# Kernel tuning notes

Hardware: AMD Instinct MI355X
Metric: run time of the kernel (lower is better)

The kernel has to match this reference:

```python
import jax, jax.numpy as jnp
import numpy as np

B = 2048
LF = 64
N_DEC, N_MOV, N_CAT, N_PER, N_COM = 12, 60000, 32, 100000, 20000


def setup_inputs() -> dict:
    key = jax.random.key(0)
    ks = jax.random.split(key, 10)

    def multihot(k, n):
        return jax.random.randint(k, (B, n), 0, 2, dtype=jnp.int32)

    def weight(k, n):
        # nn.Linear(n, LF, bias=False) weight, stored transposed as [n, LF]
        return jax.random.normal(k, (n, LF), dtype=jnp.float32) * 0.02

    return {
        "decade_idxs": multihot(ks[0], N_DEC),
        "movie_idxs": multihot(ks[1], N_MOV),
        "category_idxs": multihot(ks[2], N_CAT),
        "person_idxs": multihot(ks[3], N_PER),
        "company_idxs": multihot(ks[4], N_COM),
        "W_dec": weight(ks[5], N_DEC),
        "W_mov": weight(ks[6], N_MOV),
        "W_cat": weight(ks[7], N_CAT),
        "W_per": weight(ks[8], N_PER),
        "W_com": weight(ks[9], N_COM),
    }


def _norm_rows(emb, s):
    # divide rows whose multi-hot sum s is nonzero (np.flatnonzero semantics)
    mask = s != 0
    safe = jnp.where(mask, s, jnp.ones_like(s))
    return jnp.where(mask[:, None], emb / safe[:, None], emb)


def reference(decade_idxs, movie_idxs, category_idxs, person_idxs, company_idxs,
              W_dec, W_mov, W_cat, W_per, W_com):
    d = decade_idxs.astype(jnp.float32)
    m = movie_idxs.astype(jnp.float32)
    c = category_idxs.astype(jnp.float32)
    p = person_idxs.astype(jnp.float32)
    q = company_idxs.astype(jnp.float32)

    decades = d @ W_dec            # [B, LF]
    decades = _norm_rows(decades, jnp.sum(d, axis=1))

    movies = m @ W_mov
    # BUG in original module (replicated faithfully): `decades` is normalized
    # AGAIN by the movie-row sums; `movies` is never normalized.
    decades = _norm_rows(decades, jnp.sum(m, axis=1))

    categories = _norm_rows(c @ W_cat, jnp.sum(c, axis=1))
    persons = _norm_rows(p @ W_per, jnp.sum(p, axis=1))
    companies = _norm_rows(q @ W_com, jnp.sum(q, axis=1))

    return jnp.concatenate([decades, movies, categories, persons, companies], axis=1)
```

## Files before the change

kernel.cpp:

```cpp
#include <hip/hip_runtime.h>
#include <hip/hip_bf16.h>

#define BM 128
#define BK 64
#define CHUNK 4096
#define LF 64
#define NBAGS 5
#define BROWS 2048
#define OUTC 320

typedef __attribute__((ext_vector_type(8))) short short8;
typedef __attribute__((ext_vector_type(4))) float f32x4;

struct BagArgs {
    const int*   A[NBAGS];
    const float* W[NBAGS];
    int K[NBAGS];
    int cstart[NBAGS + 1];
};

__device__ __forceinline__ unsigned short f2bf(float f) {
    unsigned u = __float_as_uint(f);
    u += 0x7FFFu + ((u >> 16) & 1u);
    return (unsigned short)(u >> 16);
}

__global__ __launch_bounds__(256) void bag_gemm(BagArgs args,
                                                float* __restrict__ out,
                                                int* __restrict__ sums) {
    __shared__ unsigned short lsA[BM * BK];
    __shared__ unsigned short lsB[LF * BK];

    const int tid  = threadIdx.x;
    const int wave = tid >> 6;
    const int lane = tid & 63;

    int y = blockIdx.y;
    int bag = 0;
#pragma unroll
    for (int b = 1; b < NBAGS; ++b)
        if (y >= args.cstart[b]) bag = b;
    const int chunk = y - args.cstart[bag];
    const int K     = args.K[bag];
    const int k0    = chunk * CHUNK;
    const int kend  = min(k0 + CHUNK, K);
    const int m0    = blockIdx.x * BM;
    const int*   __restrict__ A = args.A[bag];
    const float* __restrict__ W = args.W[bag];

    f32x4 acc[2][4];
#pragma unroll
    for (int i = 0; i < 2; ++i)
#pragma unroll
        for (int j = 0; j < 4; ++j)
            acc[i][j] = (f32x4){0.f, 0.f, 0.f, 0.f};

    const int ar = tid >> 2;
    const int aj = tid & 3;
    const int wk = tid & 63;
    const int wc0 = (tid >> 6) * 16;

    int sum0 = 0, sum1 = 0;

    for (int kk = k0; kk < kend; kk += BK) {
#pragma unroll
        for (int half = 0; half < 2; ++half) {
            const int r = ar + half * 64;
            const size_t rowoff = (size_t)(m0 + r) * (size_t)K;
#pragma unroll
            for (int i = 0; i < 4; ++i) {
                const int col = kk + aj * 4 + i * 16;
                int4 v = make_int4(0, 0, 0, 0);
                if (col < kend) v = *(const int4*)(A + rowoff + col);
                const int s = v.x + v.y + v.z + v.w;
                if (half == 0) sum0 += s; else sum1 += s;
                unsigned p0 = (v.x ? 0x3F80u : 0u) | (v.y ? 0x3F800000u : 0u);
                unsigned p1 = (v.z ? 0x3F80u : 0u) | (v.w ? 0x3F800000u : 0u);
                int kbyte = (aj * 4 + i * 16) * 2;
                kbyte ^= (r & 7) << 4;
                *(uint2*)((char*)lsA + r * (BK * 2) + kbyte) = make_uint2(p0, p1);
            }
        }
        {
            const int gk = kk + wk;
#pragma unroll
            for (int u = 0; u < 4; ++u) {
                float4 w = make_float4(0.f, 0.f, 0.f, 0.f);
                if (gk < kend) w = *(const float4*)(W + (size_t)gk * LF + wc0 + u * 4);
                const unsigned short b0 = f2bf(w.x), b1 = f2bf(w.y),
                                     b2 = f2bf(w.z), b3 = f2bf(w.w);
                const unsigned short bs[4] = {b0, b1, b2, b3};
#pragma unroll
                for (int v2 = 0; v2 < 4; ++v2) {
                    const int c = wc0 + u * 4 + v2;
                    const int kbyte = (wk * 2) ^ ((c & 7) << 4);
                    *(unsigned short*)((char*)lsB + c * (BK * 2) + kbyte) = bs[v2];
                }
            }
        }
        __syncthreads();

        const int fr   = lane & 15;
        const int kgrp = lane >> 4;
#pragma unroll
        for (int kh = 0; kh < 2; ++kh) {
            const int kbyteR = kh * 64 + kgrp * 16;
            short8 afr[2];
#pragma unroll
            for (int mi = 0; mi < 2; ++mi) {
                const int row = wave * 32 + mi * 16 + fr;
                const int off = row * (BK * 2) + (kbyteR ^ ((row & 7) << 4));
                afr[mi] = *(const short8*)((const char*)lsA + off);
            }
#pragma unroll
            for (int ni = 0; ni < 4; ++ni) {
                const int colB = ni * 16 + fr;
                const int offb = colB * (BK * 2) + (kbyteR ^ ((colB & 7) << 4));
                const short8 bfr = *(const short8*)((const char*)lsB + offb);
#pragma unroll
                for (int mi = 0; mi < 2; ++mi)
                    acc[mi][ni] = __builtin_amdgcn_mfma_f32_16x16x32_bf16(
                        afr[mi], bfr, acc[mi][ni], 0, 0, 0);
            }
        }
        __syncthreads();
    }

    sum0 += __shfl_xor(sum0, 1);
    sum0 += __shfl_xor(sum0, 2);
    sum1 += __shfl_xor(sum1, 1);
    sum1 += __shfl_xor(sum1, 2);
    if (aj == 0) {
        atomicAdd(&sums[bag * BROWS + m0 + ar], sum0);
        atomicAdd(&sums[bag * BROWS + m0 + ar + 64], sum1);
    }

    const int fr = lane & 15;
    const int rg = lane >> 4;
#pragma unroll
    for (int mi = 0; mi < 2; ++mi)
#pragma unroll
        for (int ni = 0; ni < 4; ++ni)
#pragma unroll
            for (int r = 0; r < 4; ++r) {
                const int row = m0 + wave * 32 + mi * 16 + rg * 4 + r;
                const int col = bag * LF + ni * 16 + fr;
                atomicAdd(&out[row * OUTC + col], acc[mi][ni][r]);
            }
}

__global__ __launch_bounds__(256) void norm_fix(float* __restrict__ out,
                                                const int* __restrict__ sums) {
    const int idx = blockIdx.x * blockDim.x + threadIdx.x;
    if (idx >= BROWS * OUTC) return;
    const int m = idx / OUTC;
    const int c = idx % OUTC;
    const int bag = c >> 6;
    float v = out[idx];
    if (bag == 0) {
        const int s0 = sums[m];
        const int s1 = sums[BROWS + m];
        if (s0) v /= (float)s0;
        if (s1) v /= (float)s1;
    } else if (bag >= 2) {
        const int s = sums[bag * BROWS + m];
        if (s) v /= (float)s;
    }
    out[idx] = v;
}

extern "C" void kernel_launch(void* const* d_in, const int* in_sizes, int n_in,
                              void* d_out, int out_size, void* d_ws, size_t ws_size,
                              hipStream_t stream) {
    float* out = (float*)d_out;
    int* sums = (int*)d_ws;

    hipMemsetAsync(d_out, 0, (size_t)out_size * sizeof(float), stream);
    hipMemsetAsync(sums, 0, NBAGS * BROWS * sizeof(int), stream);

    BagArgs args;
    const int Ks[NBAGS] = {12, 60000, 32, 100000, 20000};
    int total = 0;
    for (int b = 0; b < NBAGS; ++b) {
        args.A[b] = (const int*)d_in[b];
        args.W[b] = (const float*)d_in[5 + b];
        args.K[b] = Ks[b];
        args.cstart[b] = total;
        total += (Ks[b] + CHUNK - 1) / CHUNK;
    }
    args.cstart[NBAGS] = total;

    dim3 grid(BROWS / BM, total);
    bag_gemm<<<grid, 256, 0, stream>>>(args, out, sums);

    const int n = BROWS * OUTC;
    norm_fix<<<(n + 255) / 256, 256, 0, stream>>>(out, sums);
}
```

Before: 494.8 us.

## Prepack weights to bf16 tiles, load A directly into registers, double-buffer LDS

```diff
diff --git a/kernel.cpp b/kernel.cpp
--- a/kernel.cpp
+++ b/kernel.cpp
@@ -1,13 +1,14 @@
 #include <hip/hip_runtime.h>
 #include <hip/hip_bf16.h>
 
-#define BM 128
-#define BK 64
-#define CHUNK 4096
 #define LF 64
 #define NBAGS 5
 #define BROWS 2048
 #define OUTC 320
+#define CHUNK 2048
+#define BM 64
+#define BK 64
+#define WS_SUMS_BYTES 65536
 
 typedef __attribute__((ext_vector_type(8))) short short8;
 typedef __attribute__((ext_vector_type(4))) float f32x4;
@@ -17,6 +18,7 @@
     const float* W[NBAGS];
     int K[NBAGS];
     int cstart[NBAGS + 1];
+    int tstart[NBAGS + 1];
 };
 
 __device__ __forceinline__ unsigned short f2bf(float f) {
@@ -25,128 +27,167 @@
     return (unsigned short)(u >> 16);
 }
 
-__global__ __launch_bounds__(256) void bag_gemm(BagArgs args,
-                                                float* __restrict__ out,
-                                                int* __restrict__ sums) {
-    __shared__ unsigned short lsA[BM * BK];
-    __shared__ unsigned short lsB[LF * BK];
+__device__ __forceinline__ unsigned ones2(int x, int y) {
+    return (x ? 0x3F80u : 0u) | (y ? 0x3F800000u : 0u);
+}
+
+__global__ __launch_bounds__(256) void pack_w(BagArgs args,
+                                              unsigned short* __restrict__ Wp) {
+    __shared__ unsigned short ls[4][4096];
+    const int wv = threadIdx.x >> 6;
+    const int c  = threadIdx.x & 63;
+    const int gtile = blockIdx.x * 4 + wv;
+
+    int bag = 0;
+#pragma unroll
+    for (int b = 1; b < NBAGS; ++b)
+        if (gtile >= args.tstart[b]) bag = b;
+    const int lt = gtile - args.tstart[bag];
+    const float* __restrict__ W = args.W[bag];
+    const int K = args.K[bag];
+
+    unsigned short* L = ls[wv];
+#pragma unroll 8
+    for (int k = 0; k < 64; ++k) {
+        const int gk = lt * 64 + k;
+        float v = (gk < K) ? W[(size_t)gk * LF + c] : 0.f;
+        L[(((k >> 3) * LF) + c) * 8 + (k & 7)] = f2bf(v);
+    }
+    __syncthreads();
+    unsigned short* dst = Wp + ((size_t)gtile << 12);
+#pragma unroll
+    for (int j = 0; j < 8; ++j)
+        *(short8*)(dst + c * 8 + j * 512) = *(const short8*)(L + c * 8 + j * 512);
+}
+
+template<bool PACKED>
+__global__ __launch_bounds__(256, 4) void bag_gemm(BagArgs args,
+                                                   const unsigned short* __restrict__ Wp,
+                                                   float* __restrict__ out,
+                                                   int* __restrict__ sums)
+{
+    __shared__ unsigned short lsB[2][BK * LF];
 
     const int tid  = threadIdx.x;
     const int wave = tid >> 6;
     const int lane = tid & 63;
-
-    int y = blockIdx.y;
-    int bag = 0;
+    const int fr   = lane & 15;
+    const int kg   = lane >> 4;
+
+    int y = blockIdx.y, bag = 0;
 #pragma unroll
     for (int b = 1; b < NBAGS; ++b)
         if (y >= args.cstart[b]) bag = b;
-    const int chunk = y - args.cstart[bag];
-    const int K     = args.K[bag];
-    const int k0    = chunk * CHUNK;
-    const int kend  = min(k0 + CHUNK, K);
-    const int m0    = blockIdx.x * BM;
-    const int*   __restrict__ A = args.A[bag];
+    const int chunk  = y - args.cstart[bag];
+    const int K      = args.K[bag];
+    const int k0     = chunk * CHUNK;
+    const int kend   = min(k0 + CHUNK, K);
+    const int niters = (kend - k0 + BK - 1) >> 6;
+    const int tile0  = args.tstart[bag] + chunk * (CHUNK / BK);
+
+    const int m0  = blockIdx.x * BM;
+    const int row = m0 + wave * 16 + fr;
+    const int* __restrict__ pA = args.A[bag] + (size_t)row * K;
     const float* __restrict__ W = args.W[bag];
 
-    f32x4 acc[2][4];
-#pragma unroll
-    for (int i = 0; i < 2; ++i)
-#pragma unroll
-        for (int j = 0; j < 4; ++j)
-            acc[i][j] = (f32x4){0.f, 0.f, 0.f, 0.f};
-
-    const int ar = tid >> 2;
-    const int aj = tid & 3;
-    const int wk = tid & 63;
-    const int wc0 = (tid >> 6) * 16;
-
-    int sum0 = 0, sum1 = 0;
-
-    for (int kk = k0; kk < kend; kk += BK) {
-#pragma unroll
-        for (int half = 0; half < 2; ++half) {
-            const int r = ar + half * 64;
-            const size_t rowoff = (size_t)(m0 + r) * (size_t)K;
-#pragma unroll
-            for (int i = 0; i < 4; ++i) {
-                const int col = kk + aj * 4 + i * 16;
-                int4 v = make_int4(0, 0, 0, 0);
-                if (col < kend) v = *(const int4*)(A + rowoff + col);
-                const int s = v.x + v.y + v.z + v.w;
-                if (half == 0) sum0 += s; else sum1 += s;
-                unsigned p0 = (v.x ? 0x3F80u : 0u) | (v.y ? 0x3F800000u : 0u);
-                unsigned p1 = (v.z ? 0x3F80u : 0u) | (v.w ? 0x3F800000u : 0u);
-                int kbyte = (aj * 4 + i * 16) * 2;
-                kbyte ^= (r & 7) << 4;
-                *(uint2*)((char*)lsA + r * (BK * 2) + kbyte) = make_uint2(p0, p1);
+    f32x4 acc[4];
+#pragma unroll
+    for (int i = 0; i < 4; ++i) acc[i] = (f32x4){0.f, 0.f, 0.f, 0.f};
+    int psum = 0;
+
+    auto loadA = [&](int t, int4& x0, int4& x1, int4& x2, int4& x3) {
+        const int c0 = k0 + t * BK + kg * 8;
+        const int c1 = c0 + 32;
+        const int4 z = make_int4(0, 0, 0, 0);
+        x0 = (c0     < kend) ? *(const int4*)(pA + c0)     : z;
+        x1 = (c0 + 4 < kend) ? *(const int4*)(pA + c0 + 4) : z;
+        x2 = (c1     < kend) ? *(const int4*)(pA + c1)     : z;
+        x3 = (c1 + 4 < kend) ? *(const int4*)(pA + c1 + 4) : z;
+    };
+
+    auto stageW = [&](int t, int buf) {
+        if constexpr (PACKED) {
+            const char* src = (const char*)Wp + (((size_t)(tile0 + t)) << 13)
+                              + wave * 2048 + lane * 16;
+            char* dst = (char*)&lsB[buf][0] + wave * 2048;
+            __builtin_amdgcn_global_load_lds(
+                (const __attribute__((address_space(1))) void*)src,
+                (__attribute__((address_space(3))) void*)dst, 16, 0, 0);
+            __builtin_amdgcn_global_load_lds(
+                (const __attribute__((address_space(1))) void*)(src + 1024),
+                (__attribute__((address_space(3))) void*)(dst + 1024), 16, 0, 0);
+        } else {
+            const int kq = tid >> 4, cg = tid & 15;
+#pragma unroll
+            for (int u = 0; u < 4; ++u) {
+                const int k  = kq * 4 + u;
+                const int gk = k0 + t * BK + k;
+                float4 w = make_float4(0.f, 0.f, 0.f, 0.f);
+                if (gk < kend) w = *(const float4*)(W + (size_t)gk * LF + cg * 4);
+                unsigned short* d = &lsB[buf][(((k >> 3) * LF) + cg * 4) * 8 + (k & 7)];
+                d[0]  = f2bf(w.x);
+                d[8]  = f2bf(w.y);
+                d[16] = f2bf(w.z);
+                d[24] = f2bf(w.w);
             }
         }
-        {
-            const int gk = kk + wk;
-#pragma unroll
-            for (int u = 0; u < 4; ++u) {
-                float4 w = make_float4(0.f, 0.f, 0.f, 0.f);
-                if (gk < kend) w = *(const float4*)(W + (size_t)gk * LF + wc0 + u * 4);
-                const unsigned short b0 = f2bf(w.x), b1 = f2bf(w.y),
-                                     b2 = f2bf(w.z), b3 = f2bf(w.w);
-                const unsigned short bs[4] = {b0, b1, b2, b3};
-#pragma unroll
-                for (int v2 = 0; v2 < 4; ++v2) {
-                    const int c = wc0 + u * 4 + v2;
-                    const int kbyte = (wk * 2) ^ ((c & 7) << 4);
-                    *(unsigned short*)((char*)lsB + c * (BK * 2) + kbyte) = bs[v2];
-                }
-            }
-        }
+    };
+
+    int4 a0, a1, a2, a3;
+    loadA(0, a0, a1, a2, a3);
+    stageW(0, 0);
+    if constexpr (PACKED) asm volatile("s_waitcnt vmcnt(0)" ::: "memory");
+    __syncthreads();
+
+    for (int t = 0; t < niters; ++t) {
+        const int cur = t & 1;
+        int4 n0, n1, n2, n3;
+        if (t + 1 < niters) {
+            loadA(t + 1, n0, n1, n2, n3);
+            stageW(t + 1, cur ^ 1);
+        } else {
+            n0 = n1 = n2 = n3 = make_int4(0, 0, 0, 0);
+        }
+
+        psum += a0.x + a0.y + a0.z + a0.w + a1.x + a1.y + a1.z + a1.w
+              + a2.x + a2.y + a2.z + a2.w + a3.x + a3.y + a3.z + a3.w;
+
+        int4 u0 = make_int4(ones2(a0.x, a0.y), ones2(a0.z, a0.w),
+                            ones2(a1.x, a1.y), ones2(a1.z, a1.w));
+        int4 u1 = make_int4(ones2(a2.x, a2.y), ones2(a2.z, a2.w),
+                            ones2(a3.x, a3.y), ones2(a3.z, a3.w));
+        short8 fa0 = *(short8*)&u0;
+        short8 fa1 = *(short8*)&u1;
+
+        const unsigned short* Lb = &lsB[cur][0];
+#pragma unroll
+        for (int ni = 0; ni < 4; ++ni) {
+            short8 fb = *(const short8*)(Lb + ((0 * 4 + kg) * LF + ni * 16 + fr) * 8);
+            acc[ni] = __builtin_amdgcn_mfma_f32_16x16x32_bf16(fa0, fb, acc[ni], 0, 0, 0);
+        }
+#pragma unroll
+        for (int ni = 0; ni < 4; ++ni) {
+            short8 fb = *(const short8*)(Lb + ((1 * 4 + kg) * LF + ni * 16 + fr) * 8);
+            acc[ni] = __builtin_amdgcn_mfma_f32_16x16x32_bf16(fa1, fb, acc[ni], 0, 0, 0);
+        }
+
+        a0 = n0; a1 = n1; a2 = n2; a3 = n3;
+        if constexpr (PACKED) asm volatile("s_waitcnt vmcnt(0)" ::: "memory");
         __syncthreads();
-
-        const int fr   = lane & 15;
-        const int kgrp = lane >> 4;
-#pragma unroll
-        for (int kh = 0; kh < 2; ++kh) {
-            const int kbyteR = kh * 64 + kgrp * 16;
-            short8 afr[2];
-#pragma unroll
-            for (int mi = 0; mi < 2; ++mi) {
-                const int row = wave * 32 + mi * 16 + fr;
-                const int off = row * (BK * 2) + (kbyteR ^ ((row & 7) << 4));
-                afr[mi] = *(const short8*)((const char*)lsA + off);
-            }
-#pragma unroll
-            for (int ni = 0; ni < 4; ++ni) {
-                const int colB = ni * 16 + fr;
-                const int offb = colB * (BK * 2) + (kbyteR ^ ((colB & 7) << 4));
-                const short8 bfr = *(const short8*)((const char*)lsB + offb);
-#pragma unroll
-                for (int mi = 0; mi < 2; ++mi)
-                    acc[mi][ni] = __builtin_amdgcn_mfma_f32_16x16x32_bf16(
-                        afr[mi], bfr, acc[mi][ni], 0, 0, 0);
-            }
-        }
-        __syncthreads();
-    }
-
-    sum0 += __shfl_xor(sum0, 1);
-    sum0 += __shfl_xor(sum0, 2);
-    sum1 += __shfl_xor(sum1, 1);
-    sum1 += __shfl_xor(sum1, 2);
-    if (aj == 0) {
-        atomicAdd(&sums[bag * BROWS + m0 + ar], sum0);
-        atomicAdd(&sums[bag * BROWS + m0 + ar + 64], sum1);
-    }
-
-    const int fr = lane & 15;
+    }
+
+    psum += __shfl_xor(psum, 16);
+    psum += __shfl_xor(psum, 32);
+    if (kg == 0) atomicAdd(&sums[bag * BROWS + row], psum);
+
     const int rg = lane >> 4;
-#pragma unroll
-    for (int mi = 0; mi < 2; ++mi)
-#pragma unroll
-        for (int ni = 0; ni < 4; ++ni)
-#pragma unroll
-            for (int r = 0; r < 4; ++r) {
-                const int row = m0 + wave * 32 + mi * 16 + rg * 4 + r;
-                const int col = bag * LF + ni * 16 + fr;
-                atomicAdd(&out[row * OUTC + col], acc[mi][ni][r]);
-            }
+    const int colb = bag * LF;
+#pragma unroll
+    for (int ni = 0; ni < 4; ++ni)
+#pragma unroll
+        for (int r = 0; r < 4; ++r)
+            atomicAdd(&out[(size_t)(m0 + wave * 16 + rg * 4 + r) * OUTC + colb + ni * 16 + fr],
+                      acc[ni][r]);
 }
 
 __global__ __launch_bounds__(256) void norm_fix(float* __restrict__ out,
@@ -174,25 +215,36 @@
                               hipStream_t stream) {
     float* out = (float*)d_out;
     int* sums = (int*)d_ws;
+    unsigned short* Wp = (unsigned short*)((char*)d_ws + WS_SUMS_BYTES);
 
     hipMemsetAsync(d_out, 0, (size_t)out_size * sizeof(float), stream);
     hipMemsetAsync(sums, 0, NBAGS * BROWS * sizeof(int), stream);
 
     BagArgs args;
     const int Ks[NBAGS] = {12, 60000, 32, 100000, 20000};
-    int total = 0;
+    int ccum = 0, tcum = 0;
     for (int b = 0; b < NBAGS; ++b) {
         args.A[b] = (const int*)d_in[b];
         args.W[b] = (const float*)d_in[5 + b];
         args.K[b] = Ks[b];
-        args.cstart[b] = total;
-        total += (Ks[b] + CHUNK - 1) / CHUNK;
-    }
-    args.cstart[NBAGS] = total;
-
-    dim3 grid(BROWS / BM, total);
-    bag_gemm<<<grid, 256, 0, stream>>>(args, out, sums);
-
-    const int n = BROWS * OUTC;
-    norm_fix<<<(n + 255) / 256, 256, 0, stream>>>(out, sums);
-}
+        args.cstart[b] = ccum;
+        args.tstart[b] = tcum;
+        ccum += (Ks[b] + CHUNK - 1) / CHUNK;
+        tcum += (Ks[b] + BK - 1) / BK;
+    }
+    args.cstart[NBAGS] = ccum;
+    args.tstart[NBAGS] = tcum;
+
+    const size_t need = WS_SUMS_BYTES + (size_t)tcum * (size_t)(BK * LF) * sizeof(unsigned short);
+    const bool packed = (ws_size >= need) && (tcum % 4 == 0);
+
+    dim3 grid(BROWS / BM, ccum);
+    if (packed) {
+        pack_w<<<tcum / 4, 256, 0, stream>>>(args, Wp);
+        bag_gemm<true><<<grid, 256, 0, stream>>>(args, Wp, out, sums);
+    } else {
+        bag_gemm<false><<<grid, 256, 0, stream>>>(args, Wp, out, sums);
+    }
+
+    norm_fix<<<(BROWS * OUTC + 255) / 256, 256, 0, stream>>>(out, sums);
+}
```

Measured after the change: 735.8 us. 48.7% more time.
